# Optimization experiments

Hardware: AMD Instinct MI355X
Metric: run time of the kernel (lower is better)

The kernel has to match this reference:

```python
import jax, jax.numpy as jnp
import numpy as np
from jax import lax

EPS = 1e-5  # BatchNorm eps; eval-mode BN with running_mean=0, running_var=1


def _bn(v, g, b):
    return v * (g / jnp.sqrt(1.0 + EPS)) + b


def setup_inputs() -> dict:
    key = jax.random.key(0)
    ks = jax.random.split(key, 8)
    B, I, O, H, W, E, K, r = 16, 128, 128, 128, 128, 16, 3, 8
    Ir, Or = I // r, O // r
    f = jax.random.normal
    return {
        "x": f(ks[0], (B, I, H, W), jnp.float32),
        "experts": f(ks[1], (E, O, I, K, K), jnp.float32) * 0.05,
        "rw1": f(ks[2], (Ir, I), jnp.float32) * 0.05,
        "rbn1_g": jnp.ones((Ir,), jnp.float32),
        "rbn1_b": jnp.zeros((Ir,), jnp.float32),
        "rw2": f(ks[3], (I, Ir), jnp.float32) * 0.05,
        "rbn2_g": jnp.ones((I,), jnp.float32),
        "rbn2_b": jnp.zeros((I,), jnp.float32),
        "rw3": f(ks[4], (E, I), jnp.float32) * 0.05,
        "rb3": jnp.zeros((E,), jnp.float32),
        "ca_w1": f(ks[5], (Or, O), jnp.float32) * 0.05,
        "ca_bn1_g": jnp.ones((Or,), jnp.float32),
        "ca_bn1_b": jnp.zeros((Or,), jnp.float32),
        "ca_w2": f(ks[6], (O, Or), jnp.float32) * 0.05,
        "ca_bn2_g": jnp.ones((O,), jnp.float32),
        "ca_bn2_b": jnp.zeros((O,), jnp.float32),
        "sa_w": f(ks[7], (1, 2, 7, 7), jnp.float32) * 0.05,
        "sa_bn_g": jnp.ones((1,), jnp.float32),
        "sa_bn_b": jnp.zeros((1,), jnp.float32),
    }


def reference(x, experts, rw1, rbn1_g, rbn1_b, rw2, rbn2_g, rbn2_b, rw3, rb3,
              ca_w1, ca_bn1_g, ca_bn1_b, ca_w2, ca_bn2_g, ca_bn2_b,
              sa_w, sa_bn_g, sa_bn_b):
    B, I, H, W = x.shape
    E, O, _, K, _ = experts.shape
    # --- routing: avgpool -> 1x1 conv (matmul) -> BN -> ReLU -> 1x1 -> BN -> sigmoid -> 1x1 -> softmax
    p = jnp.mean(x, axis=(2, 3))                                  # [B, I]
    h = jax.nn.relu(_bn(p @ rw1.T, rbn1_g, rbn1_b))               # [B, I/r]
    g = jax.nn.sigmoid(_bn(h @ rw2.T, rbn2_g, rbn2_b))            # [B, I]
    rweights = jax.nn.softmax(g @ rw3.T + rb3, axis=1)            # [B, E]
    # --- expert-weighted kernel generation as a single GEMM
    w = jnp.einsum('be,eoihw->boihw', rweights, experts)          # [B, O, I, K, K]
    # --- per-sample conv via grouped conv (groups = B), stride=1, padding=1
    out = lax.conv_general_dilated(
        x.reshape(1, B * I, H, W),
        w.reshape(B * O, I, K, K),
        window_strides=(1, 1), padding=((1, 1), (1, 1)),
        dimension_numbers=('NCHW', 'OIHW', 'NCHW'),
        feature_group_count=B,
    ).reshape(B, O, H, W)
    # --- SE channel attention
    cp = jnp.mean(out, axis=(2, 3))                               # [B, O]
    ch = jax.nn.relu(_bn(cp @ ca_w1.T, ca_bn1_g, ca_bn1_b))
    cw = jax.nn.sigmoid(_bn(ch @ ca_w2.T, ca_bn2_g, ca_bn2_b))    # [B, O]
    out = out * cw[:, :, None, None]
    # --- CBAM spatial attention
    sp = jnp.concatenate([jnp.mean(out, axis=1, keepdims=True),
                          jnp.max(out, axis=1, keepdims=True)], axis=1)  # [B,2,H,W]
    sw = lax.conv_general_dilated(sp, sa_w, (1, 1), ((3, 3), (3, 3)),
                                  dimension_numbers=('NCHW', 'OIHW', 'NCHW'))
    sw = jax.nn.sigmoid(_bn(sw, sa_bn_g.reshape(1, 1, 1, 1), sa_bn_b.reshape(1, 1, 1, 1)))
    out = out * sw
    # --- residual (in_channels == out_channels -> Identity)
    return out + x
```

## Files before the change

### kernel.cpp

```cpp
#include <hip/hip_runtime.h>

typedef unsigned short ushort_t;
typedef __attribute__((ext_vector_type(4))) float float4_t;
typedef __attribute__((ext_vector_type(8))) short short8_t;
typedef __attribute__((ext_vector_type(8))) unsigned short ushort8_t;
typedef __attribute__((ext_vector_type(4))) unsigned short ushort4_t;

__device__ __forceinline__ ushort_t f2bf(float f) {
    unsigned u = __builtin_bit_cast(unsigned, f);
    u = (u + 0x7fffu + ((u >> 16) & 1u)) >> 16;
    return (ushort_t)u;
}
__device__ __forceinline__ ushort_t f2h(float f) {
    return __builtin_bit_cast(unsigned short, (_Float16)f);
}
__device__ __forceinline__ float h2f(ushort_t u) {
    return (float)__builtin_bit_cast(_Float16, u);
}

__device__ __forceinline__ void gld16(const void* g, void* l) {
    __builtin_amdgcn_global_load_lds(
        (const __attribute__((address_space(1))) unsigned int*)g,
        (__attribute__((address_space(3))) unsigned int*)l, 16, 0, 0);
}


__global__ __launch_bounds__(256) void init_kernel(float* __restrict__ p,
                                                   float* __restrict__ sp,
                                                   ushort_t* __restrict__ xn,
                                                   float* __restrict__ st,
                                                   unsigned* __restrict__ wcnt,
                                                   const float* __restrict__ x) {
    int blk = blockIdx.x;
    int tid = threadIdx.x;
    if (blk >= 6381) {
        int bi = blk - 6381;
        const float* xb = x + (long)bi * 16384;
        int half = tid >> 7, t = tid & 127;
        __shared__ float red[2][2][128];
        __shared__ float corn[4];
        float rv = half ? xb[16256 + t] : xb[t];
        float cv = half ? xb[t * 128 + 127] : xb[t * 128];
        red[0][half][t] = rv;
        red[1][half][t] = cv;
        if (tid == 0)   corn[0] = rv;
        if (tid == 127) corn[1] = rv;
        if (tid == 128) corn[2] = rv;
        if (tid == 255) corn[3] = rv;
        __syncthreads();
        int wave = tid >> 6, lane = tid & 63;
        int kind = wave >> 1, hf = wave & 1;
        float s = red[kind][hf][lane] + red[kind][hf][lane + 64];
        for (int msk = 1; msk < 64; msk <<= 1) s += __shfl_xor(s, msk, 64);
        if (lane == 0) st[bi * 8 + kind * 2 + hf] = s;
        if (tid < 4) st[bi * 8 + 4 + tid] = corn[tid];
        return;
    }
    int t = blk * 256 + tid;
    if (t < 2048) { p[t] = 0.f; if (t == 0) *wcnt = 0u; return; }
    t -= 2048;
    if (t < 574592) { sp[t] = 0.f; return; }
    t -= 574592;
    if (t < 1056768) {
        int b = t / 66048;
        int r = t % 66048;
        int pix = r >> 7, i = r & 127;
        int hp, wp;
        if (pix < 130)      { hp = 0;   wp = pix; }
        else if (pix < 260) { hp = 129; wp = pix - 130; }
        else { int q = pix - 260; hp = 1 + (q >> 1); wp = (q & 1) ? 129 : 0; }
        xn[((b * 130 + hp) * 130 + wp) * 128 + i] = 0;
    }
}

__global__ __launch_bounds__(256) void transpose_kernel(const float* __restrict__ x,
                                                        ushort_t* __restrict__ xn,
                                                        float* __restrict__ p) {
    __shared__ float tile[128][65];
    int blk = blockIdx.x;
    int wt = blk & 1, h = (blk >> 1) & 127, b = blk >> 8;
    int w0 = wt * 64;
    int tid = threadIdx.x;
    int wl = tid & 63, ig = tid >> 6;
    const float* src = x + ((long)(b * 128) * 128 + h) * 128 + w0 + wl;
    #pragma unroll
    for (int i = ig; i < 128; i += 4) tile[i][wl] = src[(long)i * 16384];
    __syncthreads();
    if (tid < 128) {
        float s = 0.f;
        #pragma unroll
        for (int w = 0; w < 64; ++w) s += tile[tid][w];
        atomicAdd(&p[b * 128 + tid], s * (1.0f / 16384.0f));
    }
    int l16 = tid & 15, wq = tid >> 4;
    #pragma unroll
    for (int pass = 0; pass < 4; ++pass) {
        int w = wq + pass * 16;
        ushort8_t v;
        #pragma unroll
        for (int j = 0; j < 8; ++j) v[j] = f2bf(tile[l16 * 8 + j][w]);
        *(ushort8_t*)&xn[((b * 130 + h + 1) * 130 + (w0 + w + 1)) * 128 + l16 * 8] = v;
    }
}

__global__ __launch_bounds__(256) void wgen_kernel(const float* __restrict__ experts,
        const float* __restrict__ p, const float* __restrict__ st,
        const float* __restrict__ rw1, const float* __restrict__ g1, const float* __restrict__ b1,
        const float* __restrict__ rw2, const float* __restrict__ g2, const float* __restrict__ b2,
        const float* __restrict__ rw3, const float* __restrict__ rb3,
        const float* __restrict__ cw1, const float* __restrict__ cg1, const float* __restrict__ cb1,
        const float* __restrict__ cw2, const float* __restrict__ cg2, const float* __restrict__ cb2,
        ushort_t* __restrict__ w2, float* __restrict__ cp, float* __restrict__ cw,
        unsigned* __restrict__ wcnt) {
    int o = blockIdx.x;
    int tid = threadIdx.x;
    int lane = tid & 63, wave = tid >> 6;
    __shared__ __align__(16) float ex[16 * 1152];
    __shared__ float sg[16][128];
    __shared__ float sh[16][16];
    __shared__ float sl[16][16];
    __shared__ float rwl[16][16];
    __shared__ float cpw[4][8];
    __shared__ int lastf;

    const float* ebase = experts + (long)o * 1152;
    #pragma unroll
    for (int j = 0; j < 4; ++j) {
        int e = wave * 4 + j;
        const char* src = (const char*)(ebase + (long)e * 147456) + lane * 16;
        char* dst = (char*)&ex[e * 1152];
        #pragma unroll
        for (int k = 0; k < 5; ++k) {
            if (k < 4 || lane < 32)
                gld16(src + k * 1024, dst + k * 1024);
        }
    }

    const float bns = rsqrtf(1.0f + 1e-5f);
    {   int b = tid >> 4, j = tid & 15;
        float s = 0.f;
        for (int i = 0; i < 128; ++i) s += p[b * 128 + i] * rw1[j * 128 + i];
        s = s * (g1[j] * bns) + b1[j];
        sh[b][j] = fmaxf(s, 0.f); }
    __syncthreads();
    for (int c = 0; c < 8; ++c) {
        int idx = tid + c * 256;
        int b = idx >> 7, j = idx & 127;
        float s = 0.f;
        for (int k = 0; k < 16; ++k) s += sh[b][k] * rw2[j * 16 + k];
        s = s * (g2[j] * bns) + b2[j];
        sg[b][j] = 1.0f / (1.0f + expf(-s));
    }
    __syncthreads();
    {   int b = tid >> 4, e = tid & 15;
        float s = rb3[e];
        for (int j = 0; j < 128; ++j) s += sg[b][j] * rw3[e * 128 + j];
        sl[b][e] = s; }
    __syncthreads();
    {   int b = tid >> 4, e = tid & 15;
        float m = -1e30f;
        for (int k = 0; k < 16; ++k) m = fmaxf(m, sl[b][k]);
        float num = expf(sl[b][e] - m), den = 0.f;
        for (int k = 0; k < 16; ++k) den += expf(sl[b][k] - m);
        rwl[b][e] = num / den; }
    asm volatile("s_waitcnt vmcnt(0)" ::: "memory");
    __syncthreads();

    int i = tid & 127, half = tid >> 7;
    float acc[8][9];
    #pragma unroll
    for (int b = 0; b < 8; ++b)
        #pragma unroll
        for (int d = 0; d < 9; ++d) acc[b][d] = 0.f;
    for (int e = 0; e < 16; ++e) {
        float v[9];
        #pragma unroll
        for (int d = 0; d < 9; ++d) v[d] = ex[e * 1152 + i * 9 + d];
        #pragma unroll
        for (int b = 0; b < 8; ++b) {
            float r = rwl[half * 8 + b][e];
            #pragma unroll
            for (int d = 0; d < 9; ++d) acc[b][d] += v[d] * r;
        }
    }
    float cps[8];
    #pragma unroll
    for (int bb2 = 0; bb2 < 8; ++bb2) {
        int b = half * 8 + bb2;
        const float* sb = st + ((b << 7) + i) * 8;
        float T = p[(b << 7) + i] * 16384.f;
        float r0 = sb[0], r127 = sb[1], c0 = sb[2], c127 = sb[3];
        float x00 = sb[4], x0127 = sb[5], x1270 = sb[6], x127127 = sb[7];
        float S0 = T - r127 - c127 + x127127;
        float S1 = T - r127;
        float S2 = T - r127 - c0 + x1270;
        float S3 = T - c127;
        float S4 = T;
        float S5 = T - c0;
        float S6 = T - r0 - c127 + x0127;
        float S7 = T - r0;
        float S8 = T - r0 - c0 + x00;
        cps[bb2] = acc[bb2][0] * S0 + acc[bb2][1] * S1 + acc[bb2][2] * S2 +
                   acc[bb2][3] * S3 + acc[bb2][4] * S4 + acc[bb2][5] * S5 +
                   acc[bb2][6] * S6 + acc[bb2][7] * S7 + acc[bb2][8] * S8;
    }
    #pragma unroll
    for (int bb2 = 0; bb2 < 8; ++bb2)
        for (int msk = 1; msk < 64; msk <<= 1) cps[bb2] += __shfl_xor(cps[bb2], msk, 64);
    if (lane == 0) {
        #pragma unroll
        for (int bb2 = 0; bb2 < 8; ++bb2) cpw[wave][bb2] = cps[bb2];
    }
    #pragma unroll
    for (int b = 0; b < 8; ++b)
        #pragma unroll
        for (int d = 0; d < 9; ++d)
            w2[(((half * 8 + b) * 9 + d) << 14) + (o << 7) + i] = f2bf(acc[b][d]);
    __syncthreads();
    if (tid < 16) {
        int hf = tid >> 3, idx = tid & 7;
        float v = cpw[hf * 2][idx] + cpw[hf * 2 + 1][idx];
        __hip_atomic_store(&cp[(tid << 7) + o], v, __ATOMIC_RELAXED,
                           __HIP_MEMORY_SCOPE_AGENT);
    }

    __threadfence();
    __syncthreads();
    if (tid == 0) lastf = (atomicAdd(wcnt, 1u) == 127u) ? 1 : 0;
    __syncthreads();
    if (!lastf) return;
    __threadfence();
    for (int c = 0; c < 8; ++c) {
        int idx = tid + c * 256;
        float v = __hip_atomic_load(&cp[idx], __ATOMIC_RELAXED, __HIP_MEMORY_SCOPE_AGENT);
        sg[idx >> 7][idx & 127] = v * (1.0f / 16384.0f);
    }
    __syncthreads();
    {   int b = tid >> 4, j = tid & 15;
        float s = 0.f;
        for (int oo = 0; oo < 128; ++oo) s += sg[b][oo] * cw1[j * 128 + oo];
        s = s * (cg1[j] * bns) + cb1[j];
        sh[b][j] = fmaxf(s, 0.f); }
    __syncthreads();
    for (int c = 0; c < 8; ++c) {
        int idx = tid + c * 256;
        int b = idx >> 7, oo = idx & 127;
        float s = 0.f;
        #pragma unroll
        for (int k = 0; k < 16; ++k) s += sh[b][k] * cw2[oo * 16 + k];
        s = s * (cg2[oo] * bns) + cb2[oo];
        cw[idx] = 1.0f / (1.0f + expf(-s));
    }
}

struct __align__(16) ConvSmem {
    union {
        struct { ushort_t X[16640]; ushort_t A[4][4096]; } t;
        float c[4224];
    };
};

__global__ __launch_bounds__(256, 2) void conv_kernel(const ushort_t* __restrict__ xn,
                                                      const ushort_t* __restrict__ w2,
                                                      const float* __restrict__ cw,
                                                      ushort_t* __restrict__ outi,
                                                      float* __restrict__ sp) {
    __shared__ ConvSmem sm;
    __shared__ float scw[128];
    __shared__ float cmb[2][128];
    int bh = (blockIdx.x & 7) * 256 + (blockIdx.x >> 3);
    int b = bh >> 7, h = bh & 127;
    int tid = threadIdx.x;
    int lane = tid & 63, wave = tid >> 6;
    int wm = wave & 1, wn = wave >> 1;
    int q = lane >> 4, nl = lane & 15;

    float4_t acc[4][4];
    #pragma unroll
    for (int mi = 0; mi < 4; ++mi)
        #pragma unroll
        for (int ni = 0; ni < 4; ++ni) acc[mi][ni] = (float4_t){0.f, 0.f, 0.f, 0.f};

    const ushort_t* xbase = xn + (b * 130 + h) * 16640;
    const ushort_t* abase = w2 + (long)b * 147456;

    float cwv = 0.f;
    if (tid < 128) cwv = cw[(b << 7) + tid];

    auto stageX = [&](int dy) {
        const ushort_t* xrow = xbase + dy * 16640;
        #pragma unroll
        for (int seg = wave; seg < 33; seg += 4) {
            if (seg < 32 || lane < 32) {
                int lofs = seg * 512 + lane * 8;
                int pp = lofs >> 7;
                int jb = (lofs & 127) >> 3;
                gld16(xrow + (pp << 7) + ((jb ^ (pp & 15)) << 3), &sm.t.X[seg * 512]);
            }
        }
    };
    auto stageA = [&](int c) {
        int dy = c / 12, rem = c % 12, dx = rem >> 2, ic = rem & 3;
        const ushort_t* ab = abase + (dy * 3 + dx) * 16384 + ic * 32;
        int buf = c & 3;
        int ol = lane >> 2;
        int jsrc = (lane & 3) ^ ((ol >> 1) & 3);
        #pragma unroll
        for (int inst = 0; inst < 2; ++inst) {
            int ob = wave * 32 + inst * 16;
            gld16(ab + (ob + ol) * 128 + (jsrc << 3), &sm.t.A[buf][ob * 32]);
        }
    };

    short8_t afr[2][4], bfr[2][4];
    auto readFrag = [&](int cc) {
        int pb = cc & 1;
        int dx = (cc % 12) >> 2, ic = cc & 3;
        const ushort_t* ap = &sm.t.A[cc & 3][0];
        #pragma unroll
        for (int mi = 0; mi < 4; ++mi) {
            int o = wm * 64 + mi * 16 + nl;
            afr[pb][mi] = *(const short8_t*)&ap[(o << 5) + ((q ^ ((o >> 1) & 3)) << 3)];
        }
        #pragma unroll
        for (int ni = 0; ni < 4; ++ni) {
            int pp = wn * 64 + ni * 16 + nl + dx;
            int J = ic * 4 + q;
            bfr[pb][ni] = *(const short8_t*)&sm.t.X[(pp << 7) + ((J ^ (pp & 15)) << 3)];
        }
    };
    auto domfma = [&](int pb) {
        __builtin_amdgcn_s_setprio(1);
        #pragma unroll
        for (int mi = 0; mi < 4; ++mi)
            #pragma unroll
            for (int ni = 0; ni < 4; ++ni)
                acc[mi][ni] = __builtin_amdgcn_mfma_f32_16x16x32_bf16(
                    afr[pb][mi], bfr[pb][ni], acc[mi][ni], 0, 0, 0);
        __builtin_amdgcn_s_setprio(0);
    };

    stageX(0);
    stageA(0); stageA(1); stageA(2);
    if (tid < 128) scw[tid] = cwv;
    asm volatile("s_waitcnt vmcnt(0)" ::: "memory");
    __builtin_amdgcn_s_barrier();
    readFrag(0);

    #pragma unroll
    for (int c = 0; c < 36; ++c) {
        if (c + 3 < 36) stageA(c + 3);
        const bool bnd = (c == 11 || c == 23);
        if (!bnd && c + 1 < 36) readFrag(c + 1);
        domfma(c & 1);
        if (bnd) {
            __builtin_amdgcn_s_barrier();
            stageX(c == 11 ? 1 : 2);
            asm volatile("s_waitcnt vmcnt(0)" ::: "memory");
            __builtin_amdgcn_s_barrier();
            readFrag(c + 1);
        } else if (c < 35) {
            if (c == 33)
                asm volatile("s_waitcnt vmcnt(0)" ::: "memory");
            else if (!(c == 0 || c == 12 || c == 24 || c == 34))
                asm volatile("s_waitcnt vmcnt(2)" ::: "memory");
            __builtin_amdgcn_s_barrier();
        }
    }

    ushort_t* outb = outi + (((long)(b << 7)) << 14) + (h << 7);
    int wpx = tid & 127, g = tid >> 7;
    float wsum = 0.f, wmax = -1e30f;
    #pragma unroll
    for (int os = 0; os < 4; ++os) {
        __syncthreads();
        if (wm == (os >> 1)) {
            #pragma unroll
            for (int mi2 = 0; mi2 < 2; ++mi2) {
                int mi = (os & 1) * 2 + mi2;
                #pragma unroll
                for (int ni = 0; ni < 4; ++ni) {
                    float4_t v = acc[mi][ni];
                    int orow = mi2 * 16 + q * 4;
                    int w = wn * 64 + ni * 16 + nl;
                    #pragma unroll
                    for (int rr = 0; rr < 4; ++rr) sm.c[(orow + rr) * 132 + w] = v[rr];
                }
            }
        }
        __syncthreads();
        int row = tid >> 4, j = tid & 15;
        #pragma unroll
        for (int pass = 0; pass < 2; ++pass) {
            int r2 = pass * 16 + row;
            ushort8_t v;
            #pragma unroll
            for (int k = 0; k < 8; ++k) v[k] = f2h(sm.c[r2 * 132 + j * 8 + k]);
            *(ushort8_t*)&outb[((long)(os * 32 + r2) << 14) + j * 8] = v;
        }
        #pragma unroll
        for (int r = 0; r < 16; ++r) {
            int orow = g * 16 + r;
            float v = sm.c[orow * 132 + wpx] * scw[os * 32 + orow];
            wsum += v;
            wmax = fmaxf(wmax, v);
        }
    }
    if (g == 1) { cmb[0][wpx] = wsum; cmb[1][wpx] = wmax; }
    __syncthreads();
    if (g == 0) {
        wsum += cmb[0][wpx];
        wmax = fmaxf(wmax, cmb[1][wpx]);
        float* d = sp + b * 2 * 17956;
        d[(h + 3) * 134 + (wpx + 3)] = wsum * (1.0f / 128.0f);
        d[17956 + (h + 3) * 134 + (wpx + 3)] = wmax;
    }
}

__global__ __launch_bounds__(256) void sattn_kernel(const float* __restrict__ sp,
        const float* __restrict__ k98, const float* __restrict__ g, const float* __restrict__ bb,
        const float* __restrict__ cw, const float* __restrict__ x,
        const ushort_t* __restrict__ outi, float* __restrict__ out) {
    int b = blockIdx.x >> 7, h = blockIdx.x & 127;
    int tid = threadIdx.x;
    __shared__ float ls[2][7][134];
    __shared__ float lk[98];
    __shared__ float sws[128];
    __shared__ float scw[128];
    const float* sb = sp + b * 2 * 17956;
    for (int idx = tid; idx < 2 * 7 * 134; idx += 256) {
        int c = idx / 938, rr = idx % 938;
        int ky = rr / 134, wp = rr % 134;
        ls[c][ky][wp] = sb[c * 17956 + (h + ky) * 134 + wp];
    }
    if (tid < 98) lk[tid] = k98[tid];
    if (tid >= 128) scw[tid - 128] = cw[(b << 7) + (tid - 128)];
    __syncthreads();
    if (tid < 128) {
        float s = 0.f;
        #pragma unroll
        for (int c = 0; c < 2; ++c)
            #pragma unroll
            for (int ky = 0; ky < 7; ++ky)
                #pragma unroll
                for (int kx = 0; kx < 7; ++kx)
                    s += ls[c][ky][tid + kx] * lk[c * 49 + ky * 7 + kx];
        s = s * (g[0] * rsqrtf(1.0f + 1e-5f)) + bb[0];
        sws[tid] = 1.0f / (1.0f + expf(-s));
    }
    __syncthreads();
    int w4 = tid & 31, og = tid >> 5;
    long base = (((long)b << 21) + (h << 7)) + (w4 << 2);
    float4_t sv = *(const float4_t*)&sws[w4 << 2];
    #pragma unroll
    for (int o = og; o < 128; o += 8) {
        long idx = base + ((long)o << 14);
        ushort4_t hv = *(const ushort4_t*)&outi[idx];
        float4_t ov = (float4_t){h2f(hv[0]), h2f(hv[1]), h2f(hv[2]), h2f(hv[3])};
        float4_t xv = *(const float4_t*)&x[idx];
        float4_t r = ov * scw[o] * sv + xv;
        *(float4_t*)&out[idx] = r;
    }
}

extern "C" void kernel_launch(void* const* d_in, const int* in_sizes, int n_in,
                              void* d_out, int out_size, void* d_ws, size_t ws_size,
                              hipStream_t stream) {
    const float* x       = (const float*)d_in[0];
    const float* experts = (const float*)d_in[1];
    const float* rw1     = (const float*)d_in[2];
    const float* rbn1_g  = (const float*)d_in[3];
    const float* rbn1_b  = (const float*)d_in[4];
    const float* rw2     = (const float*)d_in[5];
    const float* rbn2_g  = (const float*)d_in[6];
    const float* rbn2_b  = (const float*)d_in[7];
    const float* rw3     = (const float*)d_in[8];
    const float* rb3     = (const float*)d_in[9];
    const float* ca_w1   = (const float*)d_in[10];
    const float* ca_bn1g = (const float*)d_in[11];
    const float* ca_bn1b = (const float*)d_in[12];
    const float* ca_w2   = (const float*)d_in[13];
    const float* ca_bn2g = (const float*)d_in[14];
    const float* ca_bn2b = (const float*)d_in[15];
    const float* sa_w    = (const float*)d_in[16];
    const float* sa_g    = (const float*)d_in[17];
    const float* sa_b    = (const float*)d_in[18];
    float* out = (float*)d_out;
    char* ws = (char*)d_ws;

    ushort_t* xn   = (ushort_t*)(ws);
    ushort_t* w2   = (ushort_t*)(ws + 69222400);
    float*    p    = (float*)(ws + 73940992);
    float*    cp   = (float*)(ws + 73949184);
    unsigned* wcnt = (unsigned*)(ws + 73957376);
    float*    cw   = (float*)(ws + 73958400);
    float*    sp   = (float*)(ws + 73966592);
    ushort_t* outi = (ushort_t*)(ws + 76264960);
    float*    st   = (float*)(ws + 143373824);

    hipLaunchKernelGGL(init_kernel, dim3(8429), dim3(256), 0, stream,
                       p, sp, xn, st, wcnt, x);
    hipLaunchKernelGGL(transpose_kernel, dim3(4096), dim3(256), 0, stream, x, xn, p);
    hipLaunchKernelGGL(wgen_kernel, dim3(128), dim3(256), 0, stream,
                       experts, p, st, rw1, rbn1_g, rbn1_b, rw2, rbn2_g, rbn2_b, rw3, rb3,
                       ca_w1, ca_bn1g, ca_bn1b, ca_w2, ca_bn2g, ca_bn2b,
                       w2, cp, cw, wcnt);
    hipLaunchKernelGGL(conv_kernel, dim3(2048), dim3(256), 0, stream, xn, w2, cw, outi, sp);
    hipLaunchKernelGGL(sattn_kernel, dim3(2048), dim3(256), 0, stream,
                       sp, sa_w, sa_g, sa_b, cw, x, outi, out);
}
```

Measured before the change: 481.0 us.

## Give each wave private double-buffered A tiles and drop per-chunk block barriers

Each wave now stages its own 64-row slice of the expert-weight tile into a private two-slot LDS buffer, replacing the shared four-slot buffer. This lets the main 36-chunk loop drop its block-wide barrier on every chunk; waves synchronise only at the X-row boundaries. The MFMA work for each chunk is split into two halves, with the next fragment read placed between them to overlap LDS reads with matrix math. In exchange, weight traffic from global memory or L2 doubles, since the two waves sharing a row slice each load it. There is also a possible hazard: the async LDS write into a slot may overlap fragment reads of that slot that have not yet completed.

```diff
diff --git a/kernel.cpp b/kernel.cpp
--- a/kernel.cpp
+++ b/kernel.cpp
@@ -255,7 +255,7 @@
 
 struct __align__(16) ConvSmem {
     union {
-        struct { ushort_t X[16640]; ushort_t A[4][4096]; } t;
+        struct { ushort_t X[16640]; ushort_t A[4][2][2048]; } t;
         float c[4224];
     };
 };
@@ -272,7 +272,7 @@
     int b = bh >> 7, h = bh & 127;
     int tid = threadIdx.x;
     int lane = tid & 63, wave = tid >> 6;
-    int wm = wave & 1, wn = wave >> 1;
+    int wm = wave >> 1, wn = wave & 1;
     int q = lane >> 4, nl = lane & 15;
 
     float4_t acc[4][4];
@@ -282,10 +282,7 @@
         for (int ni = 0; ni < 4; ++ni) acc[mi][ni] = (float4_t){0.f, 0.f, 0.f, 0.f};
 
     const ushort_t* xbase = xn + (b * 130 + h) * 16640;
-    const ushort_t* abase = w2 + (long)b * 147456;
-
-    float cwv = 0.f;
-    if (tid < 128) cwv = cw[(b << 7) + tid];
+    const ushort_t* abase = w2 + (long)b * 147456 + (wm * 64) * 128;
 
     auto stageX = [&](int dy) {
         const ushort_t* xrow = xbase + dy * 16640;
@@ -302,13 +299,13 @@
     auto stageA = [&](int c) {
         int dy = c / 12, rem = c % 12, dx = rem >> 2, ic = rem & 3;
         const ushort_t* ab = abase + (dy * 3 + dx) * 16384 + ic * 32;
-        int buf = c & 3;
+        ushort_t* dst = &sm.t.A[wave][c & 1][0];
         int ol = lane >> 2;
         int jsrc = (lane & 3) ^ ((ol >> 1) & 3);
         #pragma unroll
-        for (int inst = 0; inst < 2; ++inst) {
-            int ob = wave * 32 + inst * 16;
-            gld16(ab + (ob + ol) * 128 + (jsrc << 3), &sm.t.A[buf][ob * 32]);
+        for (int inst = 0; inst < 4; ++inst) {
+            int ob = inst * 16;
+            gld16(ab + (ob + ol) * 128 + (jsrc << 3), dst + ob * 32);
         }
     };
 
@@ -316,11 +313,11 @@
     auto readFrag = [&](int cc) {
         int pb = cc & 1;
         int dx = (cc % 12) >> 2, ic = cc & 3;
-        const ushort_t* ap = &sm.t.A[cc & 3][0];
+        const ushort_t* ap = &sm.t.A[wave][cc & 1][0];
         #pragma unroll
         for (int mi = 0; mi < 4; ++mi) {
-            int o = wm * 64 + mi * 16 + nl;
-            afr[pb][mi] = *(const short8_t*)&ap[(o << 5) + ((q ^ ((o >> 1) & 3)) << 3)];
+            int ol = mi * 16 + nl;
+            afr[pb][mi] = *(const short8_t*)&ap[(ol << 5) + ((q ^ ((ol >> 1) & 3)) << 3)];
         }
         #pragma unroll
         for (int ni = 0; ni < 4; ++ni) {
@@ -329,10 +326,10 @@
             bfr[pb][ni] = *(const short8_t*)&sm.t.X[(pp << 7) + ((J ^ (pp & 15)) << 3)];
         }
     };
-    auto domfma = [&](int pb) {
+    auto domfmaH = [&](int pb, int m0) {
         __builtin_amdgcn_s_setprio(1);
         #pragma unroll
-        for (int mi = 0; mi < 4; ++mi)
+        for (int mi = m0; mi < m0 + 2; ++mi)
             #pragma unroll
             for (int ni = 0; ni < 4; ++ni)
                 acc[mi][ni] = __builtin_amdgcn_mfma_f32_16x16x32_bf16(
@@ -341,34 +338,33 @@
     };
 
     stageX(0);
-    stageA(0); stageA(1); stageA(2);
-    if (tid < 128) scw[tid] = cwv;
+    stageA(0); stageA(1);
     asm volatile("s_waitcnt vmcnt(0)" ::: "memory");
     __builtin_amdgcn_s_barrier();
     readFrag(0);
 
     #pragma unroll
     for (int c = 0; c < 36; ++c) {
-        if (c + 3 < 36) stageA(c + 3);
+        if (c + 2 < 36) stageA(c + 2);
+        domfmaH(c & 1, 0);
         const bool bnd = (c == 11 || c == 23);
-        if (!bnd && c + 1 < 36) readFrag(c + 1);
-        domfma(c & 1);
+        if (!bnd && c + 1 < 36) {
+            if (c == 34) asm volatile("s_waitcnt vmcnt(0)" ::: "memory");
+            else         asm volatile("s_waitcnt vmcnt(4)" ::: "memory");
+            readFrag(c + 1);
+        }
+        domfmaH(c & 1, 2);
         if (bnd) {
             __builtin_amdgcn_s_barrier();
             stageX(c == 11 ? 1 : 2);
             asm volatile("s_waitcnt vmcnt(0)" ::: "memory");
             __builtin_amdgcn_s_barrier();
             readFrag(c + 1);
-        } else if (c < 35) {
-            if (c == 33)
-                asm volatile("s_waitcnt vmcnt(0)" ::: "memory");
-            else if (!(c == 0 || c == 12 || c == 24 || c == 34))
-                asm volatile("s_waitcnt vmcnt(2)" ::: "memory");
-            __builtin_amdgcn_s_barrier();
         }
     }
 
     ushort_t* outb = outi + (((long)(b << 7)) << 14) + (h << 7);
+    if (tid < 128) scw[tid] = cw[(b << 7) + tid];
     int wpx = tid & 127, g = tid >> 7;
     float wsum = 0.f, wmax = -1e30f;
     #pragma unroll
```

Measured after the change: 472.9 us. About the same (-1.7%).
